# Optimization experiments

Measured on AMD Instinct MI355X. Metric: run time of the kernel, lower is better.

Reference implementation:

```python
import jax, jax.numpy as jnp
import numpy as np

T = 2048          # tokens (flattened batch*seq, vLLM style)
HID = 2048        # hidden_size
NH = 16           # num_heads
D_NOPE = 128
D_ROPE = 64
D_QK = D_NOPE + D_ROPE   # 192
D_V = 128
Q_LORA = 1536
KV_LORA = 512
THETA = 10000.0
EPS = 1e-6
SCALING = D_QK ** -0.5


def _rmsnorm(x, g):
    return x * jax.lax.rsqrt(jnp.mean(x * x, axis=-1, keepdims=True) + EPS) * g


def _rope(pos, x):
    # interleaved (is_neox_style=False) rotary embedding
    d = x.shape[-1]
    inv = 1.0 / (THETA ** (jnp.arange(0, d, 2, dtype=jnp.float32) / d))
    f = pos.astype(jnp.float32)[:, None] * inv          # [T, d/2]
    cos, sin = jnp.cos(f), jnp.sin(f)
    for _ in range(x.ndim - 2):                          # broadcast over heads
        cos, sin = cos[:, None], sin[:, None]
    x1, x2 = x[..., 0::2], x[..., 1::2]
    o1 = x1 * cos - x2 * sin
    o2 = x1 * sin + x2 * cos
    return jnp.stack([o1, o2], axis=-1).reshape(x.shape)


def setup_inputs() -> dict:
    key = jax.random.key(0)
    ks = jax.random.split(key, 6)
    s = 0.02
    return {
        "hidden_states": jax.random.normal(ks[0], (T, HID), jnp.float32),
        "positions": jnp.arange(T, dtype=jnp.int32),
        "w_qkv_a": jax.random.normal(ks[1], (HID, Q_LORA + KV_LORA + D_ROPE), jnp.float32) * s,
        "g_q": jnp.ones((Q_LORA,), jnp.float32),
        "w_q_b": jax.random.normal(ks[2], (Q_LORA, NH * D_QK), jnp.float32) * s,
        "g_kv": jnp.ones((KV_LORA,), jnp.float32),
        "w_kv_b": jax.random.normal(ks[3], (KV_LORA, NH * (D_NOPE + D_V)), jnp.float32) * s,
        "w_o": jax.random.normal(ks[4], (NH * D_V, HID), jnp.float32) * s,
    }


def reference(hidden_states, positions, w_qkv_a, g_q, w_q_b, g_kv, w_kv_b, w_o):
    # fused low-rank a-projection: [T, q_lora + kv_lora + rope]
    qkv_a = hidden_states @ w_qkv_a
    q_lat = qkv_a[:, :Q_LORA]
    kv_lat = qkv_a[:, Q_LORA:Q_LORA + KV_LORA]
    k_pe = qkv_a[:, Q_LORA + KV_LORA:]                   # [T, rope]

    # query path: rmsnorm -> b-projection -> [T, H, d_qk]
    q = (_rmsnorm(q_lat, g_q) @ w_q_b).reshape(T, NH, D_QK)
    q_nope, q_pe = q[..., :D_NOPE], q[..., D_NOPE:]

    # kv path: rmsnorm -> b-projection -> [T, H, nope + v]
    kv = (_rmsnorm(kv_lat, g_kv) @ w_kv_b).reshape(T, NH, D_NOPE + D_V)
    k_nope, v = kv[..., :D_NOPE], kv[..., D_NOPE:]

    q_pe = _rope(positions, q_pe)                        # [T, H, rope]
    k_pe = _rope(positions, k_pe)                        # [T, rope] shared MQA rope key

    qf = jnp.concatenate([q_nope, q_pe], axis=-1)        # [T, H, d_qk]
    kf = jnp.concatenate([k_nope, jnp.broadcast_to(k_pe[:, None, :], (T, NH, D_ROPE))], axis=-1)

    scores = jnp.einsum("thd,shd->hts", qf, kf) * SCALING   # [H, T, T]
    mask = jnp.tril(jnp.ones((T, T), dtype=bool))
    scores = jnp.where(mask, scores, jnp.finfo(scores.dtype).min)
    probs = jax.nn.softmax(scores, axis=-1)
    out = jnp.einsum("hts,shd->thd", probs, v)           # [T, H, d_v]
    return out.reshape(T, NH * D_V) @ w_o                # [T, hidden]
```

## Files before the change

kernel.cpp:

```cpp
#include <hip/hip_runtime.h>
#include <hip/hip_bf16.h>
#include <math.h>

typedef __bf16 bf16_t;
typedef __bf16 bf16x8 __attribute__((ext_vector_type(8)));
typedef float floatx4 __attribute__((ext_vector_type(4)));
typedef int intx4 __attribute__((ext_vector_type(4)));

#define T_TOK 2048
#define HID 2048
#define NH 16
#define D_NOPE 128
#define D_ROPE 64
#define D_QK 192
#define D_V 128
#define Q_LORA 1536
#define KV_LORA 512
#define QKV_N 2112
#define QKV_NPAD 2176
#define SCALING 0.07216878364870323f
#define LOG2E 1.442695041f
#define EXP_C1 (SCALING * LOG2E)
#define EXP_C2 (12.0f * LOG2E)

#define MFMA_BF16(a, b, c) __builtin_amdgcn_mfma_f32_16x16x32_bf16(a, b, c, 0, 0, 0)

__device__ __forceinline__ void gload16(const void* g, void* l) {
    __builtin_amdgcn_global_load_lds(
        (const __attribute__((address_space(1))) unsigned int*)g,
        (__attribute__((address_space(3))) unsigned int*)l, 16, 0, 0);
}

template <int MODE>
__global__ __launch_bounds__(256) void gemm_mfma(
    const bf16_t* __restrict__ A, const bf16_t* __restrict__ Bt,
    float* __restrict__ Cf, bf16_t* __restrict__ Cb,
    bf16_t* __restrict__ kfull, bf16_t* __restrict__ vtmp,
    int M, int N, int K)
{
    __shared__ __align__(16) bf16_t As[2 * 128 * 32];
    __shared__ __align__(16) bf16_t Bs[2 * 128 * 32];
    const int tid = threadIdx.x;
    const int lane = tid & 63;
    const int w = tid >> 6;
    const int wm = w >> 1, wn = w & 1;
    const int m0 = blockIdx.y * 128, n0 = blockIdx.x * 128;
    const int l15 = lane & 15, quad = lane >> 4;

    floatx4 acc[4][4] = {};

    for (int k0 = 0; k0 < K; k0 += 64) {
#pragma unroll
        for (int it = 0; it < 4; ++it) {
            int slot = it * 256 + tid;
            int kk2 = slot >> 9;
            int r = (slot >> 2) & 127;
            int c = slot & 3;
            gload16((const char*)(A + (size_t)(m0 + r) * K + k0 + kk2 * 32 + c * 8),
                    (char*)As + slot * 16);
            gload16((const char*)(Bt + (size_t)(n0 + r) * K + k0 + kk2 * 32 + c * 8),
                    (char*)Bs + slot * 16);
        }
        __syncthreads();
#pragma unroll
        for (int kk2 = 0; kk2 < 2; ++kk2) {
            bf16x8 af[4], bfr[4];
#pragma unroll
            for (int mi = 0; mi < 4; ++mi)
                af[mi] = *(const bf16x8*)(As + kk2 * 4096 +
                                          (wm * 64 + mi * 16 + l15) * 32 + quad * 8);
#pragma unroll
            for (int ni = 0; ni < 4; ++ni)
                bfr[ni] = *(const bf16x8*)(Bs + kk2 * 4096 +
                                           (wn * 64 + ni * 16 + l15) * 32 + quad * 8);
#pragma unroll
            for (int mi = 0; mi < 4; ++mi)
#pragma unroll
                for (int ni = 0; ni < 4; ++ni)
                    acc[mi][ni] = MFMA_BF16(af[mi], bfr[ni], acc[mi][ni]);
        }
        __syncthreads();
    }

#pragma unroll
    for (int mi = 0; mi < 4; ++mi)
#pragma unroll
        for (int ni = 0; ni < 4; ++ni)
#pragma unroll
            for (int r = 0; r < 4; ++r) {
                int row = m0 + wm * 64 + mi * 16 + quad * 4 + r;
                int col = n0 + wn * 64 + ni * 16 + l15;
                float v = acc[mi][ni][r];
                if (MODE == 0) {
                    Cf[(size_t)row * N + col] = v;
                } else if (MODE == 1) {
                    Cb[(size_t)row * N + col] = (bf16_t)v;
                } else {
                    int h = col >> 8, dd = col & 255;
                    if (dd < 128)
                        kfull[((size_t)h * T_TOK + row) * 192 + dd] = (bf16_t)v;
                    else
                        vtmp[(size_t)row * 2048 + h * 128 + (dd - 128)] = (bf16_t)v;
                }
            }
}

__global__ void transpose_all(const float* __restrict__ w0, const float* __restrict__ w1,
                              const float* __restrict__ w2, const float* __restrict__ w3,
                              bf16_t* __restrict__ o0, bf16_t* __restrict__ o1,
                              bf16_t* __restrict__ o2, bf16_t* __restrict__ o3) {
    const float* in; bf16_t* out; int K, N;
    switch (blockIdx.z) {
        case 0: in = w0; out = o0; K = 2048; N = 2112; break;
        case 1: in = w1; out = o1; K = 1536; N = 3072; break;
        case 2: in = w2; out = o2; K = 512;  N = 4096; break;
        default: in = w3; out = o3; K = 2048; N = 2048; break;
    }
    int n0 = blockIdx.x * 32, k0 = blockIdx.y * 32;
    if (n0 >= N || k0 >= K) return;
    __shared__ float tile[32][33];
    int tx = threadIdx.x, ty = threadIdx.y;
    for (int i = ty; i < 32; i += 8)
        tile[i][tx] = in[(size_t)(k0 + i) * N + n0 + tx];
    __syncthreads();
    for (int i = ty; i < 32; i += 8)
        out[(size_t)(n0 + i) * K + k0 + tx] = (bf16_t)tile[tx][i];
}

__global__ void transpose_b2b(const bf16_t* __restrict__ in, bf16_t* __restrict__ out,
                              int R, int C) {
    __shared__ bf16_t tile[32][33];
    int c0 = blockIdx.x * 32, r0 = blockIdx.y * 32;
    int tx = threadIdx.x, ty = threadIdx.y;
    for (int i = ty; i < 32; i += 8)
        tile[i][tx] = in[(size_t)(r0 + i) * C + c0 + tx];
    __syncthreads();
    for (int i = ty; i < 32; i += 8)
        out[(size_t)(c0 + i) * R + r0 + tx] = tile[tx][i];
}

__global__ void cvt_f2b(const float* __restrict__ in, bf16_t* __restrict__ out, int n) {
    int i = blockIdx.x * 256 + threadIdx.x;
    if (i < n) out[i] = (bf16_t)in[i];
}

__global__ void mid_fuse(const float* __restrict__ qkv_a, const int* __restrict__ pos,
                         const float* __restrict__ g_q, const float* __restrict__ g_kv,
                         bf16_t* __restrict__ qn, bf16_t* __restrict__ kvn,
                         bf16_t* __restrict__ kfull) {
    int t = blockIdx.x, tid = threadIdx.x;
    const float* x = qkv_a + (size_t)t * QKV_NPAD;
    __shared__ float red[256];
    float ss = 0.f;
    for (int c = tid; c < Q_LORA; c += 256) { float v = x[c]; ss += v * v; }
    red[tid] = ss;
    __syncthreads();
    for (int o = 128; o > 0; o >>= 1) {
        if (tid < o) red[tid] += red[tid + o];
        __syncthreads();
    }
    float rq = rsqrtf(red[0] / (float)Q_LORA + 1e-6f);
    __syncthreads();
    ss = 0.f;
    for (int c = Q_LORA + tid; c < Q_LORA + KV_LORA; c += 256) { float v = x[c]; ss += v * v; }
    red[tid] = ss;
    __syncthreads();
    for (int o = 128; o > 0; o >>= 1) {
        if (tid < o) red[tid] += red[tid + o];
        __syncthreads();
    }
    float rkv = rsqrtf(red[0] / (float)KV_LORA + 1e-6f);

    for (int c = tid; c < Q_LORA; c += 256)
        qn[(size_t)t * Q_LORA + c] = (bf16_t)(x[c] * rq * g_q[c]);
    for (int c = tid; c < KV_LORA; c += 256)
        kvn[(size_t)t * KV_LORA + c] = (bf16_t)(x[Q_LORA + c] * rkv * g_kv[c]);

    if (tid < 32) {
        int i = tid;
        double inv = pow(10000.0, -(double)(2 * i) / 64.0);
        double fd = (double)pos[t] * inv;
        float c = (float)cos(fd), s = (float)sin(fd);
        float x1 = x[Q_LORA + KV_LORA + 2 * i], x2 = x[Q_LORA + KV_LORA + 2 * i + 1];
        bf16_t v0 = (bf16_t)(x1 * c - x2 * s);
        bf16_t v1 = (bf16_t)(x1 * s + x2 * c);
#pragma unroll
        for (int h = 0; h < NH; ++h) {
            kfull[((size_t)h * T_TOK + t) * 192 + 128 + 2 * i] = v0;
            kfull[((size_t)h * T_TOK + t) * 192 + 128 + 2 * i + 1] = v1;
        }
    }
}

__global__ void rope_q_kernel(bf16_t* __restrict__ q, const int* __restrict__ pos) {
    int idx = blockIdx.x * blockDim.x + threadIdx.x;
    if (idx >= T_TOK * NH * 32) return;
    int i = idx & 31;
    int h = (idx >> 5) & (NH - 1);
    int t = idx >> 9;
    double inv = pow(10000.0, -(double)(2 * i) / 64.0);
    double fd = (double)pos[t] * inv;
    float c = (float)cos(fd), s = (float)sin(fd);
    bf16_t* base = q + (size_t)t * (NH * D_QK) + h * D_QK + D_NOPE;
    float x1 = (float)base[2 * i], x2 = (float)base[2 * i + 1];
    base[2 * i] = (bf16_t)(x1 * c - x2 * s);
    base[2 * i + 1] = (bf16_t)(x1 * s + x2 * c);
}

__global__ __launch_bounds__(256, 2) void attn_part(
    const bf16_t* __restrict__ qbuf, const bf16_t* __restrict__ kfull,
    const bf16_t* __restrict__ vT,
    bf16_t* __restrict__ oP0, bf16_t* __restrict__ oP1, float* __restrict__ l_part)
{
    const int id = blockIdx.x;
    const int h = id & 15;
    const int c = (id >> 4) & 3;
    const int qt = 15 - (id >> 6);
    const int q0 = qt * 128;
    const int nTile = 2 * (qt + 1);
    const int tbase = nTile >> 2, trem = nTile & 3;
    const int sz = tbase + (c < trem ? 1 : 0);
    const int sBeg = c * tbase + (c < trem ? c : trem);
    const int sEnd = sBeg + sz;
    const int unit = qt * 16 + h;
    const int tid = threadIdx.x, lane = tid & 63, w = tid >> 6;
    const int l15 = lane & 15, quad = lane >> 4;
    const int ckey = (l15 >> 1) & 3;

    __shared__ __align__(16) bf16_t kn2[2][6 * 64 * 32];
    __shared__ __align__(16) bf16_t vt2[2 * 128 * 32];
    __shared__ __align__(16) bf16_t p_s[128 * 64];

    bf16x8 qf[2][6];
#pragma unroll
    for (int st = 0; st < 2; ++st) {
        const bf16_t* qp = qbuf + (size_t)(q0 + w * 32 + st * 16 + l15) * (NH * D_QK) +
                           h * D_QK;
#pragma unroll
        for (int kk = 0; kk < 6; ++kk)
            qf[st][kk] = *(const bf16x8*)(qp + kk * 32 + quad * 8);
    }

    bf16x8 ones;
#pragma unroll
    for (int j = 0; j < 8; ++j) ones[j] = (bf16_t)1.0f;

    floatx4 o[2][8] = {};
    floatx4 lac[2] = {};
    intx4 vreg[4];

#define STAGE_KN(buf_, s0_)                                                              \
    do {                                                                                 \
        _Pragma("unroll")                                                                \
        for (int it = 0; it < 6; ++it) {                                                 \
            int slot = it * 256 + tid;                                                   \
            int kk = slot >> 8, s = (slot >> 2) & 63, cc = slot & 3;                     \
            int cs = cc ^ ((s >> 1) & 3);                                                \
            gload16((const char*)(kfull + ((size_t)h * T_TOK + (s0_) + s) * 192 +        \
                                  kk * 32 + cs * 8),                                     \
                    (char*)kn2[buf_] + slot * 16);                                       \
        }                                                                                \
    } while (0)

#define VLOAD(s0_)                                                                       \
    do {                                                                                 \
        _Pragma("unroll")                                                                \
        for (int it = 0; it < 4; ++it) {                                                 \
            int slot = it * 256 + tid;                                                   \
            int ks = slot >> 9, d = (slot >> 2) & 127, cc = slot & 3;                    \
            vreg[it] = *(const intx4*)(vT + ((size_t)h * 128 + d) * T_TOK + (s0_) +      \
                                       ks * 32 + cc * 8);                                \
        }                                                                                \
    } while (0)

#define VWRITE()                                                                         \
    do {                                                                                 \
        _Pragma("unroll")                                                                \
        for (int it = 0; it < 4; ++it) {                                                 \
            int slot = it * 256 + tid;                                                   \
            int ks = slot >> 9, d = (slot >> 2) & 127, cc = slot & 3;                    \
            *(intx4*)((char*)vt2 +                                                       \
                      (size_t)((ks * 512 + d * 4 + (cc ^ ((d >> 1) & 3))) * 16)) =       \
                vreg[it];                                                                \
        }                                                                                \
    } while (0)

    if (sz > 0) {
        VLOAD(sBeg * 64);
        STAGE_KN(0, sBeg * 64);
        VWRITE();
    }

    for (int si = sBeg; si < sEnd; ++si) {
        const int s0 = si * 64;
        const int buf = (si - sBeg) & 1;
        __syncthreads();
        if (si + 1 < sEnd) {
            VLOAD(s0 + 64);
            STAGE_KN(buf ^ 1, s0 + 64);
        }

        floatx4 s_acc[2][4] = {};
        __builtin_amdgcn_s_setprio(1);
#pragma unroll
        for (int ni = 0; ni < 4; ++ni) {
#pragma unroll
            for (int kk = 0; kk < 6; ++kk) {
                bf16x8 b = *(const bf16x8*)(kn2[buf] + kk * 2048 +
                                            (ni * 16 + l15) * 32 + (quad ^ ckey) * 8);
                s_acc[0][ni] = MFMA_BF16(qf[0][kk], b, s_acc[0][ni]);
                s_acc[1][ni] = MFMA_BF16(qf[1][kk], b, s_acc[1][ni]);
            }
        }
        __builtin_amdgcn_s_setprio(0);

        const bool diag = (si >= 2 * qt);
#pragma unroll
        for (int st = 0; st < 2; ++st)
#pragma unroll
            for (int ni = 0; ni < 4; ++ni)
#pragma unroll
                for (int r = 0; r < 4; ++r) {
                    int prow = w * 32 + st * 16 + quad * 4 + r;
                    int pcol = ni * 16 + l15;
                    float pv = exp2f(s_acc[st][ni][r] * EXP_C1 - EXP_C2);
                    if (diag && (s0 + pcol) > (q0 + prow)) pv = 0.f;
                    p_s[prow * 64 + ((((pcol >> 3) ^ (prow & 7))) << 3) + (pcol & 7)] =
                        (bf16_t)pv;
                }

        __builtin_amdgcn_s_setprio(1);
#pragma unroll
        for (int ks = 0; ks < 2; ++ks) {
            bf16x8 a0, a1;
            {
                int arow = w * 32 + l15;
                a0 = *(const bf16x8*)(p_s + arow * 64 +
                                      (((ks * 4 + quad) ^ (arow & 7)) << 3));
                arow += 16;
                a1 = *(const bf16x8*)(p_s + arow * 64 +
                                      (((ks * 4 + quad) ^ (arow & 7)) << 3));
            }
            lac[0] = MFMA_BF16(a0, ones, lac[0]);
            lac[1] = MFMA_BF16(a1, ones, lac[1]);
#pragma unroll
            for (int ni = 0; ni < 8; ++ni) {
                bf16x8 b = *(const bf16x8*)(vt2 + ks * 4096 +
                                            (ni * 16 + l15) * 32 + (quad ^ ckey) * 8);
                o[0][ni] = MFMA_BF16(a0, b, o[0][ni]);
                o[1][ni] = MFMA_BF16(a1, b, o[1][ni]);
            }
        }
        __builtin_amdgcn_s_setprio(0);

        __syncthreads();
        if (si + 1 < sEnd) VWRITE();
    }

    bf16_t* op = ((c < 2) ? oP0 : oP1) + (size_t)(unit * 2 + (c & 1)) * 128 * 128;
#pragma unroll
    for (int st = 0; st < 2; ++st) {
#pragma unroll
        for (int ni = 0; ni < 8; ++ni)
#pragma unroll
            for (int r = 0; r < 4; ++r) {
                int lrow = w * 32 + st * 16 + quad * 4 + r;
                op[(size_t)lrow * 128 + ni * 16 + l15] = (bf16_t)o[st][ni][r];
            }
        if (l15 == 0)
#pragma unroll
            for (int r = 0; r < 4; ++r) {
                int lrow = w * 32 + st * 16 + quad * 4 + r;
                l_part[((size_t)unit * 4 + c) * 128 + lrow] = lac[st][r];
            }
    }
#undef STAGE_KN
#undef VLOAD
#undef VWRITE
}

__global__ void attn_combine(const bf16_t* __restrict__ oP0,
                             const bf16_t* __restrict__ oP1,
                             const float* __restrict__ l_part,
                             bf16_t* __restrict__ attn_o)
{
    int idx = blockIdx.x * 256 + threadIdx.x;
    int t = idx >> 8, cg = idx & 255;
    int col = cg * 8;
    int h = col >> 7, d = col & 127;
    int qt = t >> 7, lrow = t & 127;
    size_t unit = (size_t)qt * 16 + h;
    const float* lp = l_part + unit * 4 * 128 + lrow;
    float inv = 1.f / (lp[0] + lp[128] + lp[256] + lp[384]);
    size_t r0 = ((unit * 2 + 0) * 128 + lrow) * 128 + d;
    size_t r1 = ((unit * 2 + 1) * 128 + lrow) * 128 + d;
    bf16x8 a0 = *(const bf16x8*)(oP0 + r0);
    bf16x8 a1 = *(const bf16x8*)(oP0 + r1);
    bf16x8 a2 = *(const bf16x8*)(oP1 + r0);
    bf16x8 a3 = *(const bf16x8*)(oP1 + r1);
    bf16x8 out;
#pragma unroll
    for (int j = 0; j < 8; ++j)
        out[j] = (bf16_t)(((float)a0[j] + (float)a1[j] + (float)a2[j] + (float)a3[j]) * inv);
    *(bf16x8*)(attn_o + (size_t)t * (NH * D_V) + col) = out;
}

extern "C" void kernel_launch(void* const* d_in, const int* in_sizes, int n_in,
                              void* d_out, int out_size, void* d_ws, size_t ws_size,
                              hipStream_t stream) {
    const float* hidden = (const float*)d_in[0];
    const int* positions = (const int*)d_in[1];
    const float* w_qkv_a = (const float*)d_in[2];
    const float* g_q = (const float*)d_in[3];
    const float* w_q_b = (const float*)d_in[4];
    const float* g_kv = (const float*)d_in[5];
    const float* w_kv_b = (const float*)d_in[6];
    const float* w_o = (const float*)d_in[7];
    float* out = (float*)d_out;

    char* p = (char*)d_ws;
    float* qkv_a = (float*)p;
    bf16_t* attn_o = (bf16_t*)p;
    p += (size_t)T_TOK * QKV_NPAD * 4;
    bf16_t* hbf = (bf16_t*)p;
    bf16_t* qn = hbf;
    bf16_t* kvn = hbf + (size_t)T_TOK * Q_LORA;
    p += (size_t)T_TOK * HID * 2;
    bf16_t* qbuf = (bf16_t*)p;  p += (size_t)T_TOK * NH * D_QK * 2;
    bf16_t* vtmp = (bf16_t*)p;  p += (size_t)T_TOK * NH * D_V * 2;
    bf16_t* kfull = (bf16_t*)p; p += (size_t)NH * T_TOK * 192 * 2;
    bf16_t* vT = (bf16_t*)p;    p += (size_t)NH * 128 * T_TOK * 2;
    bf16_t* wt_qkv_a = (bf16_t*)p; p += (size_t)QKV_NPAD * HID * 2;
    bf16_t* wt_q_b = (bf16_t*)p;   p += (size_t)3072 * Q_LORA * 2;
    bf16_t* wt_kv_b = (bf16_t*)p;  p += (size_t)4096 * KV_LORA * 2;
    bf16_t* wt_o = (bf16_t*)p;

    bf16_t* oP0 = wt_qkv_a;
    bf16_t* oP1 = (bf16_t*)((char*)d_ws + (size_t)T_TOK * HID * 2);
    float* l_part = (float*)vtmp;

    dim3 tb(32, 8);

    cvt_f2b<<<(T_TOK * HID) / 256, 256, 0, stream>>>(hidden, hbf, T_TOK * HID);
    transpose_all<<<dim3(128, 64, 4), tb, 0, stream>>>(
        w_qkv_a, w_q_b, w_kv_b, w_o, wt_qkv_a, wt_q_b, wt_kv_b, wt_o);

    gemm_mfma<0><<<dim3(QKV_NPAD / 128, T_TOK / 128), 256, 0, stream>>>(
        hbf, wt_qkv_a, qkv_a, nullptr, nullptr, nullptr, T_TOK, QKV_NPAD, HID);

    mid_fuse<<<T_TOK, 256, 0, stream>>>(qkv_a, positions, g_q, g_kv, qn, kvn, kfull);

    gemm_mfma<1><<<dim3(3072 / 128, T_TOK / 128), 256, 0, stream>>>(
        qn, wt_q_b, nullptr, qbuf, nullptr, nullptr, T_TOK, 3072, Q_LORA);
    rope_q_kernel<<<(T_TOK * NH * 32) / 256, 256, 0, stream>>>(qbuf, positions);

    gemm_mfma<2><<<dim3(4096 / 128, T_TOK / 128), 256, 0, stream>>>(
        kvn, wt_kv_b, nullptr, nullptr, kfull, vtmp, T_TOK, 4096, KV_LORA);
    transpose_b2b<<<dim3(HID / 32, T_TOK / 32), tb, 0, stream>>>(vtmp, vT, T_TOK, HID);

    attn_part<<<1024, 256, 0, stream>>>(qbuf, kfull, vT, oP0, oP1, l_part);
    attn_combine<<<(T_TOK * 256) / 256, 256, 0, stream>>>(oP0, oP1, l_part, attn_o);

    gemm_mfma<0><<<dim3(HID / 128, T_TOK / 128), 256, 0, stream>>>(
        attn_o, wt_o, out, nullptr, nullptr, nullptr, T_TOK, HID, NH * D_V);
}
```

Measured before the change: 362.9 us.

## Double-buffer LDS tiles in MFMA GEMM to overlap loads with compute

The GEMM kernel now keeps two LDS buffers for the A and B tiles. It issues the async global-to-LDS loads for the next k-step before computing on the current one, which also removes the second barrier in each iteration. The goal is to hide global load latency behind the MFMA work. In exchange, LDS use per block doubles to 64 KB, which may lower occupancy.

```diff
diff --git a/kernel.cpp b/kernel.cpp
--- a/kernel.cpp
+++ b/kernel.cpp
@@ -38,8 +38,8 @@
     bf16_t* __restrict__ kfull, bf16_t* __restrict__ vtmp,
     int M, int N, int K)
 {
-    __shared__ __align__(16) bf16_t As[2 * 128 * 32];
-    __shared__ __align__(16) bf16_t Bs[2 * 128 * 32];
+    __shared__ __align__(16) bf16_t As[2][2 * 128 * 32];
+    __shared__ __align__(16) bf16_t Bs[2][2 * 128 * 32];
     const int tid = threadIdx.x;
     const int lane = tid & 63;
     const int w = tid >> 6;
@@ -49,29 +49,36 @@
 
     floatx4 acc[4][4] = {};
 
+#define GSTAGE(db_, k0_)                                                                 \
+    do {                                                                                 \
+        _Pragma("unroll")                                                                \
+        for (int it = 0; it < 4; ++it) {                                                 \
+            int slot = it * 256 + tid;                                                   \
+            int kk2 = slot >> 9;                                                         \
+            int r = (slot >> 2) & 127;                                                   \
+            int c = slot & 3;                                                            \
+            gload16((const char*)(A + (size_t)(m0 + r) * K + (k0_) + kk2 * 32 + c * 8),  \
+                    (char*)As[db_] + slot * 16);                                         \
+            gload16((const char*)(Bt + (size_t)(n0 + r) * K + (k0_) + kk2 * 32 + c * 8), \
+                    (char*)Bs[db_] + slot * 16);                                         \
+        }                                                                                \
+    } while (0)
+
+    GSTAGE(0, 0);
+    int db = 0;
     for (int k0 = 0; k0 < K; k0 += 64) {
-#pragma unroll
-        for (int it = 0; it < 4; ++it) {
-            int slot = it * 256 + tid;
-            int kk2 = slot >> 9;
-            int r = (slot >> 2) & 127;
-            int c = slot & 3;
-            gload16((const char*)(A + (size_t)(m0 + r) * K + k0 + kk2 * 32 + c * 8),
-                    (char*)As + slot * 16);
-            gload16((const char*)(Bt + (size_t)(n0 + r) * K + k0 + kk2 * 32 + c * 8),
-                    (char*)Bs + slot * 16);
-        }
         __syncthreads();
+        if (k0 + 64 < K) GSTAGE(db ^ 1, k0 + 64);
 #pragma unroll
         for (int kk2 = 0; kk2 < 2; ++kk2) {
             bf16x8 af[4], bfr[4];
 #pragma unroll
             for (int mi = 0; mi < 4; ++mi)
-                af[mi] = *(const bf16x8*)(As + kk2 * 4096 +
+                af[mi] = *(const bf16x8*)(As[db] + kk2 * 4096 +
                                           (wm * 64 + mi * 16 + l15) * 32 + quad * 8);
 #pragma unroll
             for (int ni = 0; ni < 4; ++ni)
-                bfr[ni] = *(const bf16x8*)(Bs + kk2 * 4096 +
+                bfr[ni] = *(const bf16x8*)(Bs[db] + kk2 * 4096 +
                                            (wn * 64 + ni * 16 + l15) * 32 + quad * 8);
 #pragma unroll
             for (int mi = 0; mi < 4; ++mi)
@@ -79,8 +86,9 @@
                 for (int ni = 0; ni < 4; ++ni)
                     acc[mi][ni] = MFMA_BF16(af[mi], bfr[ni], acc[mi][ni]);
         }
-        __syncthreads();
-    }
+        db ^= 1;
+    }
+#undef GSTAGE
 
 #pragma unroll
     for (int mi = 0; mi < 4; ++mi)
```

Result: faster. 349.6 us (-3.7%).
